# Optimization experiments

Measured on AMD Instinct MI355X. Metric: run time of the kernel, lower is better.

The kernel has to match this reference:

```python
import jax, jax.numpy as jnp
import numpy as np

HEADS = 16
LN_EPS = 1e-5

def setup_inputs() -> dict:
    key = jax.random.key(0)
    ks = jax.random.split(key, 8)
    B, S, NT = 4, 1024, 1024
    sc = 1.0 / np.sqrt(NT)
    return {
        "x": jax.random.normal(ks[0], (B, S, NT), dtype=jnp.float32),
        "Wq": jax.random.normal(ks[1], (NT, NT), dtype=jnp.float32) * sc,
        "bq": jax.random.normal(ks[2], (NT,), dtype=jnp.float32) * 0.02,
        "Wk": jax.random.normal(ks[3], (NT, NT), dtype=jnp.float32) * sc,
        "bk": jax.random.normal(ks[4], (NT,), dtype=jnp.float32) * 0.02,
        "Wv": jax.random.normal(ks[5], (NT, NT), dtype=jnp.float32) * sc,
        "bv": jax.random.normal(ks[6], (NT,), dtype=jnp.float32) * 0.02,
        "gamma": jnp.ones((NT,), dtype=jnp.float32),
        "beta": jnp.zeros((NT,), dtype=jnp.float32),
    }

def reference(x, Wq, bq, Wk, bk, Wv, bv, gamma, beta):
    B, S, nt = x.shape
    heads = HEADS
    dph = nt // heads
    # torch nn.Linear: y = x @ W.T + b
    q = x @ Wq.T + bq
    k = x @ Wk.T + bk
    v = x @ Wv.T + bv
    # torch .view(B*heads, -1, dph) is a row-major reshape (interleaved split)
    q = q.reshape(B * heads, -1, dph)
    k = k.reshape(B * heads, -1, dph)
    v = v.reshape(B * heads, -1, dph)
    # scaled scores; scale uses last dim of the score matrix (== seq len here)
    att = jnp.einsum('bid,bjd->bij', q, k)
    scale = att.shape[-1] ** (-0.5)
    att = jax.nn.softmax(jax.nn.relu(att * scale), axis=-1)
    # dropout in eval mode -> identity
    at_sum_sum = att.sum(axis=1).reshape(B, heads, -1)  # [B, heads, S]
    context = jnp.einsum('bij,bjd->bid', att, v).reshape(B, -1, nt)
    h = x + context
    mu = h.mean(axis=-1, keepdims=True)
    var = h.var(axis=-1, keepdims=True)
    out = (h - mu) * jax.lax.rsqrt(var + LN_EPS) * gamma + beta
    return out, at_sum_sum
```

## Files before the change

### kernel.cpp

```cpp
#include <hip/hip_runtime.h>
#include <hip/hip_bf16.h>
#include <cstdint>
#include <cstddef>


typedef short short8 __attribute__((ext_vector_type(8)));
typedef short short4v __attribute__((ext_vector_type(4)));
typedef float f32x4 __attribute__((ext_vector_type(4)));

#define MFMA32(a, b, c) __builtin_amdgcn_mfma_f32_16x16x32_bf16(a, b, c, 0, 0, 0)
#define MFMA16x16(a, b, c) __builtin_amdgcn_mfma_f32_16x16x16bf16_1k(a, b, c, 0, 0, 0)
#define ATT_SCALE 0.03125f

__device__ __forceinline__ short f2bf(float f) {
  union { float f; uint32_t u; } x; x.f = f;
  uint32_t u = x.u + 0x7fffu + ((x.u >> 16) & 1u);
  return (short)(u >> 16);
}

__device__ __forceinline__ uint32_t pk_bf16_trunc(float lo, float hi) {
  return __builtin_amdgcn_perm(__float_as_uint(hi), __float_as_uint(lo),
                               0x07060302u);
}

#define GLDS16(gp, lp)                                                        \
  __builtin_amdgcn_global_load_lds(                                           \
      (const __attribute__((address_space(1))) void*)(gp),                    \
      (__attribute__((address_space(3))) void*)(lp), 16, 0, 0)
#define GLDS4(gp, lp)                                                         \
  __builtin_amdgcn_global_load_lds(                                           \
      (const __attribute__((address_space(1))) void*)(gp),                    \
      (__attribute__((address_space(3))) void*)(lp), 4, 0, 0)

__global__ __launch_bounds__(256) void convert_kernel(
    const float* __restrict__ x, const float* __restrict__ wq,
    const float* __restrict__ wk, const float* __restrict__ wv,
    short* __restrict__ xb, short* __restrict__ wb) {
  const long XN = 4L * 1024 * 1024, WN = 1024L * 1024;
  long e = (long)(blockIdx.x * blockDim.x + threadIdx.x) * 4;
  const float* src; short* dst;
  if (e < XN)               { src = x  + e;                dst = xb + e; }
  else if (e < XN + WN)     { src = wq + (e - XN);         dst = wb + (e - XN); }
  else if (e < XN + 2 * WN) { src = wk + (e - XN - WN);    dst = wb + (e - XN); }
  else                      { src = wv + (e - XN - 2*WN);  dst = wb + (e - XN); }
  f32x4 v = *(const f32x4*)src;
  short4v o;
  o[0] = f2bf(v[0]); o[1] = f2bf(v[1]); o[2] = f2bf(v[2]); o[3] = f2bf(v[3]);
  *(short4v*)dst = o;
}

__global__ __launch_bounds__(256, 3) void qkv_gemm(
    const short* __restrict__ xb, const short* __restrict__ wb,
    const float* __restrict__ bq, const float* __restrict__ bk,
    const float* __restrict__ bv, short* __restrict__ qb,
    short* __restrict__ kb, short* __restrict__ vtp) {
  __shared__ short As[128 * 32];
  __shared__ short Bs[128 * 32];
  const int tid = threadIdx.x;
  const int lane = tid & 63;
  const int lm = lane & 15, quad = lane >> 4;
  const int wave = tid >> 6, wy = wave >> 1, wx = wave & 1;
  const int f = blockIdx.x + (blockIdx.y << 3);
  const int r8 = f & 7, s = f >> 3;
  const int m0 = (((r8 >> 1) << 3) + (s & 7)) * 128;
  const int n0 = (((r8 & 1) << 2) + (s >> 3)) * 128;
  const int z = blockIdx.z;
  const short* w = wb + (size_t)z * (1024 * 1024);
  const float* bias = (z == 0) ? bq : (z == 1) ? bk : bv;
  const float scl = (z == 0) ? ATT_SCALE : 1.0f;

  const short* gA0 = xb + (size_t)(m0 + (tid >> 2)) * 1024 + (tid & 3) * 8;
  const short* gA1 = gA0 + 64 * 1024;
  const short* gB0 = w  + (size_t)(n0 + (tid >> 2)) * 1024 + (tid & 3) * 8;
  const short* gB1 = gB0 + 64 * 1024;
  short* lA0 = As + tid * 8;
  short* lA1 = As + (tid + 256) * 8;
  short* lB0 = Bs + tid * 8;
  short* lB1 = Bs + (tid + 256) * 8;

  f32x4 acc[4][4];
#pragma unroll
  for (int i = 0; i < 4; i++)
#pragma unroll
    for (int j = 0; j < 4; j++) acc[i][j] = (f32x4){0.f, 0.f, 0.f, 0.f};

  for (int k0 = 0; k0 < 1024; k0 += 32) {
    GLDS16(gA0 + k0, lA0);
    GLDS16(gA1 + k0, lA1);
    GLDS16(gB0 + k0, lB0);
    GLDS16(gB1 + k0, lB1);
    __syncthreads();
    short8 a[4], b[4];
#pragma unroll
    for (int t = 0; t < 4; t++)
      a[t] = *(const short8*)(As + (wy * 64 + t * 16 + lm) * 32 + quad * 8);
#pragma unroll
    for (int t = 0; t < 4; t++)
      b[t] = *(const short8*)(Bs + (wx * 64 + t * 16 + lm) * 32 + quad * 8);
#pragma unroll
    for (int mt = 0; mt < 4; mt++)
#pragma unroll
      for (int nt = 0; nt < 4; nt++)
        acc[mt][nt] = MFMA32(a[mt], b[nt], acc[mt][nt]);
    __syncthreads();
  }
  if (z == 2) {
#pragma unroll
    for (int nt = 0; nt < 4; nt++) {
      const int n = n0 + wx * 64 + nt * 16 + lm;
      const float bn = bias[n];
      const size_t nbase = (size_t)((n >> 4) & 3) * 16384 +
                           (size_t)((((n >> 8) & 3) * 16 + (n & 15)) * 4 +
                                    ((n >> 6) & 3));
#pragma unroll
      for (int mt = 0; mt < 4; mt++) {
#pragma unroll
        for (int r = 0; r < 4; r++) {
          const int m = m0 + wy * 64 + mt * 16 + quad * 4 + r;
          vtp[(size_t)(m >> 6) * 65536 + nbase + (size_t)(m & 63) * 256] =
              f2bf(acc[mt][nt][r] + bn);
        }
      }
    }
  } else {
    short* out = (z == 0) ? qb : kb;
#pragma unroll
    for (int nt = 0; nt < 4; nt++) {
      const int n = n0 + wx * 64 + nt * 16 + lm;
      const float bn = bias[n];
#pragma unroll
      for (int mt = 0; mt < 4; mt++) {
        const int mb = m0 + wy * 64 + mt * 16 + quad * 4;
#pragma unroll
        for (int r = 0; r < 4; r++)
          out[(size_t)(mb + r) * 1024 + n] = f2bf((acc[mt][nt][r] + bn) * scl);
      }
    }
  }
}

__global__ __launch_bounds__(256, 2) void attn_kernel(
    const short* __restrict__ qb, const short* __restrict__ kb,
    const short* __restrict__ vtp, const float* __restrict__ x,
    const float* __restrict__ gamma, const float* __restrict__ beta,
    float* __restrict__ out1, float* __restrict__ rvW) {
  __shared__ short Ks[3][64 * 64];
  __shared__ short Vs[3][4 * 4 * 256];

  const int tid = threadIdx.x;
  const int lane = tid & 63, wave = tid >> 6;
  const int lm = lane & 15, quad = lane >> 4;
  const int bid = blockIdx.x;
  const int h = ((bid >> 6) << 3) + (bid & 7);
  const int bb = (bid >> 3) & 7;
  const short* Qh = qb + (size_t)h * 65536;
  const short* Kh = kb + (size_t)h * 65536;
  const short* Vp = vtp + (size_t)h * 65536;
  const int i0 = bb * 128 + wave * 32;

  const short8 qA0 = *(const short8*)(Qh + (size_t)(i0 + lm) * 64 + quad * 8);
  const short8 qA1 = *(const short8*)(Qh + (size_t)(i0 + lm) * 64 + 32 + quad * 8);
  const short8 qB0 = *(const short8*)(Qh + (size_t)(i0 + 16 + lm) * 64 + quad * 8);
  const short8 qB1 = *(const short8*)(Qh + (size_t)(i0 + 16 + lm) * 64 + 32 + quad * 8);

  const int c0 = tid, c1 = tid + 256;
  const short* gK0 = Kh + (size_t)(c0 >> 3) * 64 + ((c0 & 7) ^ ((c0 >> 3) & 7)) * 8;
  const short* gK1 = Kh + (size_t)(c1 >> 3) * 64 + ((c1 & 7) ^ ((c1 >> 3) & 7)) * 8;
  const short* gV0 = Vp + (c0 >> 7) * 16384 + ((c0 >> 5) & 3) * 256 + (c0 & 31) * 8;
  const short* gV1 = Vp + (c1 >> 7) * 16384 + ((c1 >> 5) & 3) * 256 + (c1 & 31) * 8;
  const int lK0 = c0 * 8, lK1 = c1 * 8;

#define ATTN_STAGE(c, buf)                                                    \
  do {                                                                        \
    const int ko_ = ((c) & 15) * 4096, vo_ = ((c) & 15) * 1024;               \
    GLDS16(gK0 + ko_, &Ks[buf][0] + lK0);                                     \
    GLDS16(gK1 + ko_, &Ks[buf][0] + lK1);                                     \
    GLDS16(gV0 + vo_, &Vs[buf][0] + lK0);                                     \
    GLDS16(gV1 + vo_, &Vs[buf][0] + lK1);                                     \
  } while (0)

  f32x4 accA[4], accB[4];
#pragma unroll
  for (int t = 0; t < 4; t++) {
    accA[t] = (f32x4){0.f, 0.f, 0.f, 0.f};
    accB[t] = (f32x4){0.f, 0.f, 0.f, 0.f};
  }
  float dsA[4] = {0.f, 0.f, 0.f, 0.f};
  float dsB[4] = {0.f, 0.f, 0.f, 0.f};

  const int swz0 = (quad ^ (lm & 7)) * 8;
  const int swz1 = ((quad + 4) ^ (lm & 7)) * 8;

  ATTN_STAGE(0, 0);
  ATTN_STAGE(1, 1);

  for (int ch = 0; ch < 16; ch++) {
    const int b = ch % 3, bs = (ch + 2) % 3;
    asm volatile("s_waitcnt vmcnt(4)" ::: "memory");
    __builtin_amdgcn_s_barrier();
#pragma unroll
    for (int jj = 0; jj < 4; jj++) {
      const short* krow = &Ks[b][(jj * 16 + lm) * 64];
      const short8 kf0 = *(const short8*)(krow + swz0);
      const short8 kf1 = *(const short8*)(krow + swz1);
      f32x4 zA = {0.f, 0.f, 0.f, 0.f};
      zA = MFMA32(kf0, qA0, zA);
      zA = MFMA32(kf1, qA1, zA);
      f32x4 zB = {0.f, 0.f, 0.f, 0.f};
      zB = MFMA32(kf0, qB0, zB);
      zB = MFMA32(kf1, qB1, zB);
      float pA[4], pB[4];
#pragma unroll
      for (int r = 0; r < 4; r++) {
        pA[r] = __expf(fmaxf(zA[r], 0.f));
        dsA[r] += pA[r];
        pB[r] = __expf(fmaxf(zB[r], 0.f));
        dsB[r] += pB[r];
      }
      union { uint32_t u[2]; short4v s; } puA, puB;
      puA.u[0] = pk_bf16_trunc(pA[0], pA[1]);
      puA.u[1] = pk_bf16_trunc(pA[2], pA[3]);
      puB.u[0] = pk_bf16_trunc(pB[0], pB[1]);
      puB.u[1] = pk_bf16_trunc(pB[2], pB[3]);
      const short* vbase = &Vs[b][jj * 256 + lane * 4];
#pragma unroll
      for (int dt = 0; dt < 4; dt++) {
        const short4v vtf = *(const short4v*)(vbase + dt * 1024);
        accA[dt] = MFMA16x16(vtf, puA.s, accA[dt]);
        accB[dt] = MFMA16x16(vtf, puB.s, accB[dt]);
      }
    }
    if (ch < 15) ATTN_STAGE(ch + 2, bs);
  }
  asm volatile("s_waitcnt vmcnt(0)" ::: "memory");

  float tA = (dsA[0] + dsA[1]) + (dsA[2] + dsA[3]);
  tA += __shfl_xor(tA, 16);
  tA += __shfl_xor(tA, 32);
  float tB = (dsB[0] + dsB[1]) + (dsB[2] + dsB[3]);
  tB += __shfl_xor(tB, 16);
  tB += __shfl_xor(tB, 32);
  const float rvA = 1.f / tA;
  const float rvB = 1.f / tB;
  if (lane < 16) {
    rvW[h * 1024 + i0 + lm] = rvA;
    rvW[h * 1024 + i0 + 16 + lm] = rvB;
  }

  const int mA = h * 64 + bb * 8 + wave * 2;
  const int nb = lm * 64 + quad * 4;
#pragma unroll
  for (int tile = 0; tile < 2; tile++) {
    const int m = mA + tile;
    const f32x4* accT = tile ? accB : accA;
    const float rv = tile ? rvB : rvA;
    const float* xr = x + (size_t)m * 1024;
    float hv[4][4], s1 = 0.f, s2 = 0.f;
#pragma unroll
    for (int dt = 0; dt < 4; dt++) {
      f32x4 xv = *(const f32x4*)(xr + nb + dt * 16);
#pragma unroll
      for (int r = 0; r < 4; r++) {
        const float v = xv[r] + accT[dt][r] * rv;
        hv[dt][r] = v; s1 += v; s2 += v * v;
      }
    }
#pragma unroll
    for (int mk = 1; mk < 64; mk <<= 1) {
      s1 += __shfl_xor(s1, mk);
      s2 += __shfl_xor(s2, mk);
    }
    const float mu = s1 * (1.f / 1024.f);
    const float var = s2 * (1.f / 1024.f) - mu * mu;
    const float rstd = rsqrtf(var + 1e-5f);
    float* orow = out1 + (size_t)m * 1024;
#pragma unroll
    for (int dt = 0; dt < 4; dt++) {
      f32x4 gv = *(const f32x4*)(gamma + nb + dt * 16);
      f32x4 bv2 = *(const f32x4*)(beta + nb + dt * 16);
      f32x4 ov;
#pragma unroll
      for (int r = 0; r < 4; r++)
        ov[r] = (hv[dt][r] - mu) * rstd * gv[r] + bv2[r];
      *(f32x4*)(orow + nb + dt * 16) = ov;
    }
  }
}

__global__ __launch_bounds__(256, 2) void colsum_kernel(
    const short* __restrict__ qb, const short* __restrict__ kb,
    const float* __restrict__ rvW, float* __restrict__ out2) {
  __shared__ short Qs[3][64 * 64];
  __shared__ float rvS[3][64];

  const int tid = threadIdx.x;
  const int lane = tid & 63, wave = tid >> 6;
  const int lm = lane & 15, quad = lane >> 4;
  const int bid = blockIdx.x;
  const int h = ((bid >> 6) << 3) + (bid & 7);
  const int jb = (bid >> 3) & 7;
  const int j0 = jb * 128 + wave * 32;
  const short* Qh = qb + (size_t)h * 65536;
  const short* Kh = kb + (size_t)h * 65536;
  const float* rvh = rvW + h * 1024;

  const short* krA = Kh + (size_t)(j0 + lm) * 64 + quad * 8;
  const short8 kA0 = *(const short8*)krA;
  const short8 kA1 = *(const short8*)(krA + 32);
  const short* krB = Kh + (size_t)(j0 + 16 + lm) * 64 + quad * 8;
  const short8 kB0 = *(const short8*)krB;
  const short8 kB1 = *(const short8*)(krB + 32);

  const int c0 = tid, c1 = tid + 256;
  const short* gQ0 = Qh + (size_t)(c0 >> 3) * 64 + ((c0 & 7) ^ ((c0 >> 3) & 7)) * 8;
  const short* gQ1 = Qh + (size_t)(c1 >> 3) * 64 + ((c1 & 7) ^ ((c1 >> 3) & 7)) * 8;
  const int lQ0 = c0 * 8, lQ1 = c1 * 8;

#define CS_STAGE(c, buf)                                                      \
  do {                                                                        \
    const int qo_ = ((c) & 15) * 4096;                                        \
    GLDS16(gQ0 + qo_, &Qs[buf][0] + lQ0);                                     \
    GLDS16(gQ1 + qo_, &Qs[buf][0] + lQ1);                                     \
    GLDS4(rvh + ((c) & 15) * 64 + lane, &rvS[buf][0]);                        \
  } while (0)

  const int swz0 = (quad ^ (lm & 7)) * 8;
  const int swz1 = ((quad + 4) ^ (lm & 7)) * 8;

  f32x4 csA = {0.f, 0.f, 0.f, 0.f};
  f32x4 csB = {0.f, 0.f, 0.f, 0.f};

  CS_STAGE(0, 0);
  CS_STAGE(1, 1);

  for (int ch = 0; ch < 16; ch++) {
    const int b = ch % 3, bs = (ch + 2) % 3;
    asm volatile("s_waitcnt vmcnt(3)" ::: "memory");
    __builtin_amdgcn_s_barrier();
#pragma unroll
    for (int ii = 0; ii < 4; ii++) {
      const short* qrow = &Qs[b][(ii * 16 + lm) * 64];
      const short8 qf0 = *(const short8*)(qrow + swz0);
      const short8 qf1 = *(const short8*)(qrow + swz1);
      f32x4 zA = {0.f, 0.f, 0.f, 0.f};
      zA = MFMA32(kA0, qf0, zA);
      zA = MFMA32(kA1, qf1, zA);
      f32x4 zB = {0.f, 0.f, 0.f, 0.f};
      zB = MFMA32(kB0, qf0, zB);
      zB = MFMA32(kB1, qf1, zB);
      const float rvv = rvS[b][ii * 16 + lm];
#pragma unroll
      for (int r = 0; r < 4; r++) {
        csA[r] += __expf(fmaxf(zA[r], 0.f)) * rvv;
        csB[r] += __expf(fmaxf(zB[r], 0.f)) * rvv;
      }
    }
    if (ch < 15) CS_STAGE(ch + 2, bs);
  }
  asm volatile("s_waitcnt vmcnt(0)" ::: "memory");

#pragma unroll
  for (int mk = 1; mk < 16; mk <<= 1)
#pragma unroll
    for (int r = 0; r < 4; r++) {
      csA[r] += __shfl_xor(csA[r], mk);
      csB[r] += __shfl_xor(csB[r], mk);
    }
  if (lm == 0) {
    *(f32x4*)(out2 + h * 1024 + j0 + quad * 4) = csA;
    *(f32x4*)(out2 + h * 1024 + j0 + 16 + quad * 4) = csB;
  }
}

extern "C" void kernel_launch(void* const* d_in, const int* in_sizes, int n_in,
                              void* d_out, int out_size, void* d_ws, size_t ws_size,
                              hipStream_t stream) {
  const float* x  = (const float*)d_in[0];
  const float* Wq = (const float*)d_in[1];
  const float* bq = (const float*)d_in[2];
  const float* Wk = (const float*)d_in[3];
  const float* bk = (const float*)d_in[4];
  const float* Wv = (const float*)d_in[5];
  const float* bv = (const float*)d_in[6];
  const float* gamma = (const float*)d_in[7];
  const float* beta  = (const float*)d_in[8];

  float* out1 = (float*)d_out;
  float* out2 = out1 + 4L * 1024 * 1024;

  short* xb = (short*)d_ws;
  short* wb = xb + 4L * 1024 * 1024;
  short* qb = wb + 3L * 1024 * 1024;
  short* kb = qb + 4L * 1024 * 1024;
  short* vtp = kb + 4L * 1024 * 1024;
  float* rvW = (float*)wb;

  convert_kernel<<<7168, 256, 0, stream>>>(x, Wq, Wk, Wv, xb, wb);
  qkv_gemm<<<dim3(8, 32, 3), 256, 0, stream>>>(xb, wb, bq, bk, bv, qb, kb, vtp);
  attn_kernel<<<512, 256, 0, stream>>>(qb, kb, vtp, x, gamma, beta, out1, rvW);
  colsum_kernel<<<512, 256, 0, stream>>>(qb, kb, rvW, out2);
}
```

Baseline: 168.9 us.

## Deepen GEMM K-tile with swizzled LDS, split colsum over query halves, add setprio

The QKV GEMM now loads 64-wide K tiles into a swizzled LDS layout. This halves the number of barriers per K and is meant to avoid LDS bank conflicts. The colsum kernel is split into two blocks per column tile, each covering half the query chunks, with results combined by atomicAdd into an output that the convert kernel zeroes first. Occupancy is raised to 4 waves. Both attention loops also wrap their MFMA sections in s_setprio. The colsum split doubles parallelism but adds atomics, and the larger LDS tile raises shared memory use per GEMM block.

After: 165.3 us. -2.2%, faster.

```diff
diff --git a/kernel.cpp b/kernel.cpp
--- a/kernel.cpp
+++ b/kernel.cpp
@@ -35,7 +35,13 @@
 __global__ __launch_bounds__(256) void convert_kernel(
     const float* __restrict__ x, const float* __restrict__ wq,
     const float* __restrict__ wk, const float* __restrict__ wv,
-    short* __restrict__ xb, short* __restrict__ wb) {
+    short* __restrict__ xb, short* __restrict__ wb,
+    float* __restrict__ out2) {
+  if (blockIdx.x >= 7168) {
+    const int idx = (blockIdx.x - 7168) * 256 + threadIdx.x;
+    *(f32x4*)(out2 + (size_t)idx * 4) = (f32x4){0.f, 0.f, 0.f, 0.f};
+    return;
+  }
   const long XN = 4L * 1024 * 1024, WN = 1024L * 1024;
   long e = (long)(blockIdx.x * blockDim.x + threadIdx.x) * 4;
   const float* src; short* dst;
@@ -54,8 +60,8 @@
     const float* __restrict__ bq, const float* __restrict__ bk,
     const float* __restrict__ bv, short* __restrict__ qb,
     short* __restrict__ kb, short* __restrict__ vtp) {
-  __shared__ short As[128 * 32];
-  __shared__ short Bs[128 * 32];
+  __shared__ short As[128 * 64];
+  __shared__ short Bs[128 * 64];
   const int tid = threadIdx.x;
   const int lane = tid & 63;
   const int lm = lane & 15, quad = lane >> 4;
@@ -69,14 +75,12 @@
   const float* bias = (z == 0) ? bq : (z == 1) ? bk : bv;
   const float scl = (z == 0) ? ATT_SCALE : 1.0f;
 
-  const short* gA0 = xb + (size_t)(m0 + (tid >> 2)) * 1024 + (tid & 3) * 8;
-  const short* gA1 = gA0 + 64 * 1024;
-  const short* gB0 = w  + (size_t)(n0 + (tid >> 2)) * 1024 + (tid & 3) * 8;
-  const short* gB1 = gB0 + 64 * 1024;
-  short* lA0 = As + tid * 8;
-  short* lA1 = As + (tid + 256) * 8;
-  short* lB0 = Bs + tid * 8;
-  short* lB1 = Bs + (tid + 256) * 8;
+  const int srow = tid >> 3;
+  const int schk = (tid & 7) ^ (srow & 7);
+  const short* gA = xb + (size_t)(m0 + srow) * 1024 + schk * 8;
+  const short* gB = w  + (size_t)(n0 + srow) * 1024 + schk * 8;
+  short* lA = As + tid * 8;
+  short* lB = Bs + tid * 8;
 
   f32x4 acc[4][4];
 #pragma unroll
@@ -84,24 +88,28 @@
 #pragma unroll
     for (int j = 0; j < 4; j++) acc[i][j] = (f32x4){0.f, 0.f, 0.f, 0.f};
 
-  for (int k0 = 0; k0 < 1024; k0 += 32) {
-    GLDS16(gA0 + k0, lA0);
-    GLDS16(gA1 + k0, lA1);
-    GLDS16(gB0 + k0, lB0);
-    GLDS16(gB1 + k0, lB1);
+  for (int k0 = 0; k0 < 1024; k0 += 64) {
+#pragma unroll
+    for (int q = 0; q < 4; q++) {
+      GLDS16(gA + k0 + q * 32 * 1024, lA + q * 2048);
+      GLDS16(gB + k0 + q * 32 * 1024, lB + q * 2048);
+    }
     __syncthreads();
-    short8 a[4], b[4];
-#pragma unroll
-    for (int t = 0; t < 4; t++)
-      a[t] = *(const short8*)(As + (wy * 64 + t * 16 + lm) * 32 + quad * 8);
-#pragma unroll
-    for (int t = 0; t < 4; t++)
-      b[t] = *(const short8*)(Bs + (wx * 64 + t * 16 + lm) * 32 + quad * 8);
-#pragma unroll
-    for (int mt = 0; mt < 4; mt++)
-#pragma unroll
-      for (int nt = 0; nt < 4; nt++)
-        acc[mt][nt] = MFMA32(a[mt], b[nt], acc[mt][nt]);
+#pragma unroll
+    for (int ks = 0; ks < 2; ks++) {
+      const int ck = (((ks << 2) + quad) ^ (lm & 7)) * 8;
+      short8 a[4], b[4];
+#pragma unroll
+      for (int t = 0; t < 4; t++) {
+        a[t] = *(const short8*)(As + (wy * 64 + t * 16 + lm) * 64 + ck);
+        b[t] = *(const short8*)(Bs + (wx * 64 + t * 16 + lm) * 64 + ck);
+      }
+#pragma unroll
+      for (int mt = 0; mt < 4; mt++)
+#pragma unroll
+        for (int nt = 0; nt < 4; nt++)
+          acc[mt][nt] = MFMA32(a[mt], b[nt], acc[mt][nt]);
+    }
     __syncthreads();
   }
   if (z == 2) {
@@ -198,6 +206,7 @@
     const int b = ch % 3, bs = (ch + 2) % 3;
     asm volatile("s_waitcnt vmcnt(4)" ::: "memory");
     __builtin_amdgcn_s_barrier();
+    __builtin_amdgcn_s_setprio(1);
 #pragma unroll
     for (int jj = 0; jj < 4; jj++) {
       const short* krow = &Ks[b][(jj * 16 + lm) * 64];
@@ -230,6 +239,7 @@
         accB[dt] = MFMA16x16(vtf, puB.s, accB[dt]);
       }
     }
+    __builtin_amdgcn_s_setprio(0);
     if (ch < 15) ATTN_STAGE(ch + 2, bs);
   }
   asm volatile("s_waitcnt vmcnt(0)" ::: "memory");
@@ -287,7 +297,7 @@
   }
 }
 
-__global__ __launch_bounds__(256, 2) void colsum_kernel(
+__global__ __launch_bounds__(256, 4) void colsum_kernel(
     const short* __restrict__ qb, const short* __restrict__ kb,
     const float* __restrict__ rvW, float* __restrict__ out2) {
   __shared__ short Qs[3][64 * 64];
@@ -297,8 +307,10 @@
   const int lane = tid & 63, wave = tid >> 6;
   const int lm = lane & 15, quad = lane >> 4;
   const int bid = blockIdx.x;
-  const int h = ((bid >> 6) << 3) + (bid & 7);
+  const int h = ((bid >> 7) << 3) + (bid & 7);
   const int jb = (bid >> 3) & 7;
+  const int ih = (bid >> 6) & 1;
+  const int cb = ih * 8;
   const int j0 = jb * 128 + wave * 32;
   const short* Qh = qb + (size_t)h * 65536;
   const short* Kh = kb + (size_t)h * 65536;
@@ -330,13 +342,14 @@
   f32x4 csA = {0.f, 0.f, 0.f, 0.f};
   f32x4 csB = {0.f, 0.f, 0.f, 0.f};
 
-  CS_STAGE(0, 0);
-  CS_STAGE(1, 1);
-
-  for (int ch = 0; ch < 16; ch++) {
+  CS_STAGE(cb, 0);
+  CS_STAGE(cb + 1, 1);
+
+  for (int ch = 0; ch < 8; ch++) {
     const int b = ch % 3, bs = (ch + 2) % 3;
     asm volatile("s_waitcnt vmcnt(3)" ::: "memory");
     __builtin_amdgcn_s_barrier();
+    __builtin_amdgcn_s_setprio(1);
 #pragma unroll
     for (int ii = 0; ii < 4; ii++) {
       const short* qrow = &Qs[b][(ii * 16 + lm) * 64];
@@ -355,7 +368,8 @@
         csB[r] += __expf(fmaxf(zB[r], 0.f)) * rvv;
       }
     }
-    if (ch < 15) CS_STAGE(ch + 2, bs);
+    __builtin_amdgcn_s_setprio(0);
+    if (ch < 7) CS_STAGE((cb + ch + 2) & 15, bs);
   }
   asm volatile("s_waitcnt vmcnt(0)" ::: "memory");
 
@@ -367,8 +381,13 @@
       csB[r] += __shfl_xor(csB[r], mk);
     }
   if (lm == 0) {
-    *(f32x4*)(out2 + h * 1024 + j0 + quad * 4) = csA;
-    *(f32x4*)(out2 + h * 1024 + j0 + 16 + quad * 4) = csB;
+    float* pA = out2 + h * 1024 + j0 + quad * 4;
+    float* pB = pA + 16;
+#pragma unroll
+    for (int r = 0; r < 4; r++) {
+      atomicAdd(pA + r, csA[r]);
+      atomicAdd(pB + r, csB[r]);
+    }
   }
 }
 
@@ -395,8 +414,8 @@
   short* vtp = kb + 4L * 1024 * 1024;
   float* rvW = (float*)wb;
 
-  convert_kernel<<<7168, 256, 0, stream>>>(x, Wq, Wk, Wv, xb, wb);
+  convert_kernel<<<7232, 256, 0, stream>>>(x, Wq, Wk, Wv, xb, wb, out2);
   qkv_gemm<<<dim3(8, 32, 3), 256, 0, stream>>>(xb, wb, bq, bk, bv, qb, kb, vtp);
   attn_kernel<<<512, 256, 0, stream>>>(qb, kb, vtp, x, gamma, beta, out1, rvW);
-  colsum_kernel<<<512, 256, 0, stream>>>(qb, kb, rvW, out2);
-}
+  colsum_kernel<<<1024, 256, 0, stream>>>(qb, kb, rvW, out2);
+}
```
